# Performance work log

Measured on AMD Instinct MI355X. Metric: run time of the kernel, lower is better.

The kernel has to match this reference:

```python
import jax, jax.numpy as jnp
import numpy as np

P, N, C_IN = 30000, 64, 4     # pillars, max points per pillar, raw point features
OUT = 64                      # PFN output channels (must equal N for the original BN call)
C_AUG = C_IN + 5              # +3 cluster offsets, +2 center offsets
VX, VY = 0.2, 0.2
X_OFF = VX / 2 + 0.0          # pc_range x_min = 0
Y_OFF = VY / 2 + (-40.0)      # pc_range y_min = -40
EPS = 1e-3                    # BatchNorm eps from change_default_args


def setup_inputs() -> dict:
    key = jax.random.key(0)
    k1, k2, k3, k4, k5, k6 = jax.random.split(key, 6)
    features = jax.random.normal(k1, (P, N, C_IN), jnp.float32)
    num_points = jax.random.randint(k2, (P,), 1, N + 1, jnp.int32)  # >=1 to avoid div-by-zero
    coors = jax.random.randint(k3, (P, 4), 0, 352, jnp.int32)
    W = jax.random.normal(k4, (OUT, C_AUG), jnp.float32) * 0.1      # Linear(bias=False)
    gamma = 1.0 + 0.1 * jax.random.normal(k5, (OUT,), jnp.float32)  # BN weight
    beta = 0.1 * jax.random.normal(k6, (OUT,), jnp.float32)         # BN bias
    return {"features": features, "num_points": num_points, "coors": coors,
            "W": W, "gamma": gamma, "beta": beta}


def reference(features, num_points, coors, W, gamma, beta):
    dt = features.dtype
    npts = num_points.astype(dt)[:, None, None]                     # [P,1,1]
    xyz = features[:, :, :3]
    points_mean = xyz.sum(axis=1, keepdims=True) / npts             # [P,1,3]
    f_cluster = xyz - points_mean                                   # [P,N,3]
    cx = features[:, :, 0] - (coors[:, 3].astype(dt)[:, None] * VX + X_OFF)
    cy = features[:, :, 1] - (coors[:, 2].astype(dt)[:, None] * VY + Y_OFF)
    f_center = jnp.stack([cx, cy], axis=-1)                         # [P,N,2]
    feat = jnp.concatenate([features, f_cluster, f_center], axis=-1)  # [P,N,9]
    mask = (num_points[:, None] > jnp.arange(N, dtype=num_points.dtype))  # [P,N]
    feat = feat * mask[..., None].astype(dt)
    x = jnp.einsum('pnc,oc->pno', feat, W)                          # [P,N,OUT]
    # Faithful to the original: BatchNorm1d(OUT) applied WITHOUT permute, so the
    # channel axis is dim=1 (size N == OUT); training-mode batch stats over (P, last).
    mu = x.mean(axis=(0, 2), keepdims=True)                         # [1,N,1]
    var = x.var(axis=(0, 2), keepdims=True)                         # biased var, as BN
    x = (x - mu) * jax.lax.rsqrt(var + EPS) * gamma[None, :, None] + beta[None, :, None]
    x = jax.nn.relu(x)
    return x.max(axis=1)                                            # [P,OUT] (squeeze of keepdim max)
```

## Files before the change

kernel.cpp:

```cpp
#include <hip/hip_runtime.h>
#include <hip/hip_bf16.h>
#include <math.h>

typedef __attribute__((ext_vector_type(8))) __bf16 bf16x8;
typedef __attribute__((ext_vector_type(4))) float f32x4;

constexpr float VX_ = 0.2f;
constexpr float VY_ = 0.2f;
constexpr float X_OFF_ = 0.1f;
constexpr float Y_OFF_ = -39.9f;
constexpr float EPS_ = 1e-3f;

__device__ __forceinline__ float wave_sum(float v) {
#pragma unroll
  for (int off = 32; off; off >>= 1) v += __shfl_xor(v, off);
  return v;
}

__device__ __forceinline__ ushort bf16bits(float x) {
  __hip_bfloat16 h = __float2bfloat16(x);
  return __builtin_bit_cast(ushort, h);
}

__device__ __forceinline__ uint32_t cvtpk(float lo, float hi) {
  uint32_t r;
  asm("v_cvt_pk_bf16_f32 %0, %1, %2" : "=v"(r) : "v"(lo), "v"(hi));
  return r;
}

__global__ __launch_bounds__(256) void k0_prep(const float* __restrict__ W,
                                               float* __restrict__ gws,
                                               uint32_t* __restrict__ Bpack) {
  const int t = threadIdx.x;
  if (t < 180) {
    const int pr = t >> 2, k = t & 3;
    int c = 0, rem = pr;
    while (rem >= 9 - c) {
      rem -= 9 - c;
      ++c;
    }
    const int c2 = c + rem;
    float s = 0.f;
    for (int o = k * 16; o < k * 16 + 16; ++o) s += W[o * 9 + c] * W[o * 9 + c2];
    s += __shfl_xor(s, 1);
    s += __shfl_xor(s, 2);
    if (k == 0) gws[pr] = (c == c2) ? s : 2.f * s;
  } else if (t < 216) {
    const int tt = t - 180, c = tt >> 2, k = tt & 3;
    float s = 0.f;
    for (int o = k * 16; o < k * 16 + 16; ++o) s += W[o * 9 + c];
    s += __shfl_xor(s, 1);
    s += __shfl_xor(s, 2);
    if (k == 0) gws[45 + c] = s;
  }
  {
    const int nt = t >> 6, lane = t & 63;
    const int l16 = lane & 15, g16 = lane >> 4;
    const int col = nt * 16 + l16;
    ushort h[8];
#pragma unroll
    for (int j = 0; j < 8; ++j) {
      const int kk = 8 * g16 + j;
      h[j] = (kk < 9) ? bf16bits(W[col * 9 + kk]) : (ushort)0;
    }
    uint4 q;
    q.x = (uint)h[0] | ((uint)h[1] << 16);
    q.y = (uint)h[2] | ((uint)h[3] << 16);
    q.z = (uint)h[4] | ((uint)h[5] << 16);
    q.w = (uint)h[6] | ((uint)h[7] << 16);
    *reinterpret_cast<uint4*>(Bpack + (size_t)t * 4) = q;
  }
}

__global__ __launch_bounds__(256) void k1_moments(
    const float* __restrict__ feats, const int* __restrict__ npts_arr,
    const int* __restrict__ coors, const float* __restrict__ gwsbuf,
    float* __restrict__ partials, float* __restrict__ aux, int S, int P) {
  __shared__ float2 red[4][64];
  const int t = threadIdx.x, lane = t & 63, wv = t >> 6;
  float g[45], wsv[9];
#pragma unroll
  for (int i = 0; i < 45; ++i) g[i] = gwsbuf[i];
#pragma unroll
  for (int i = 0; i < 9; ++i) wsv[i] = gwsbuf[45 + i];

  float s1 = 0.f, s2 = 0.f;
  const int nw = S * 4;
  int p = blockIdx.x * 4 + wv;
  if (p < P) {
    float4 f =
        *reinterpret_cast<const float4*>(feats + (size_t)p * 256 + lane * 4);
    int np = npts_arr[p];
    int cx = coors[p * 4 + 3], cy = coors[p * 4 + 2];
    while (true) {
      const int p2 = p + nw;
      const bool has2 = p2 < P;
      float4 f2 = make_float4(0.f, 0.f, 0.f, 0.f);
      int np2 = 1, cx2 = 0, cy2 = 0;
      if (has2) {
        f2 = *reinterpret_cast<const float4*>(feats + (size_t)p2 * 256 +
                                              lane * 4);
        np2 = npts_arr[p2];
        cx2 = coors[p2 * 4 + 3];
        cy2 = coors[p2 * 4 + 2];
      }
      const float ox = (float)cx * VX_ + X_OFF_;
      const float oy = (float)cy * VY_ + Y_OFF_;
      const float inv = 1.f / (float)np;
      const float m0 = wave_sum(f.x) * inv;
      const float m1 = wave_sum(f.y) * inv;
      const float m2 = wave_sum(f.z) * inv;
      if (lane == 0) {
        *reinterpret_cast<float4*>(aux + (size_t)p * 8) =
            make_float4(m0, m1, m2, ox);
        *reinterpret_cast<float4*>(aux + (size_t)p * 8 + 4) =
            make_float4(oy, __int_as_float(np), 0.f, 0.f);
      }
      const bool valid = lane < np;
      float ft[9] = {f.x,      f.y,      f.z,      f.w,      f.x - m0,
                     f.y - m1, f.z - m2, f.x - ox, f.y - oy};
#pragma unroll
      for (int c = 0; c < 9; ++c) ft[c] = valid ? ft[c] : 0.f;
      int idx = 0;
      float t1 = 0.f, t2 = 0.f;
#pragma unroll
      for (int c = 0; c < 9; ++c) {
        float u = 0.f;
#pragma unroll
        for (int c2 = c; c2 < 9; ++c2) u = fmaf(g[idx++], ft[c2], u);
        t2 = fmaf(ft[c], u, t2);
        t1 = fmaf(ft[c], wsv[c], t1);
      }
      s1 += t1;
      s2 += t2;
      if (!has2) break;
      p = p2;
      f = f2;
      np = np2;
      cx = cx2;
      cy = cy2;
    }
  }
  red[wv][lane] = make_float2(s1, s2);
  __syncthreads();
  if (t < 64) {
    const float v = red[0][t].x + red[1][t].x + red[2][t].x + red[3][t].x;
    partials[((size_t)t * 2 + 0) * S + blockIdx.x] = v;
  } else if (t < 128) {
    const int n = t - 64;
    const float v = red[0][n].y + red[1][n].y + red[2][n].y + red[3][n].y;
    partials[((size_t)n * 2 + 1) * S + blockIdx.x] = v;
  }
}

__global__ __launch_bounds__(256) void k2_stats(
    const float* __restrict__ partials, const float* __restrict__ gamma,
    const float* __restrict__ beta, float* __restrict__ ab, int S, int P) {
  const int n = blockIdx.x, t = threadIdx.x;
  __shared__ float r1[4], r2[4];
  const float* p1 = partials + ((size_t)n * 2 + 0) * S;
  const float* p2 = partials + ((size_t)n * 2 + 1) * S;
  float a1 = 0.f, a2 = 0.f;
  for (int b = t; b < S; b += 256) {
    a1 += p1[b];
    a2 += p2[b];
  }
  a1 = wave_sum(a1);
  a2 = wave_sum(a2);
  const int wv = t >> 6;
  if ((t & 63) == 0) {
    r1[wv] = a1;
    r2[wv] = a2;
  }
  __syncthreads();
  if (t == 0) {
    const float v2 = r1[0] + r1[1] + r1[2] + r1[3];
    const float v1 = r2[0] + r2[1] + r2[2] + r2[3];
    const float invPN = 1.f / ((float)P * 64.f);
    const float mu = v2 * invPN;
    const float var = v1 * invPN - mu * mu;
    const float a = gamma[n] * rsqrtf(var + EPS_);
    const float b = beta[n] - mu * a;
    ab[n] = a;
    ab[64 + n] = b;
  }
}

__global__ __launch_bounds__(256) void k4_mfma(
    const float* __restrict__ feats, const float* __restrict__ aux,
    const uint32_t* __restrict__ Bpack, const float* __restrict__ ab,
    float* __restrict__ out, int P) {
  __shared__ uint32_t A_lds[4][64][20];
  __shared__ float2 shab[64];
  const int t = threadIdx.x, lane = t & 63, wv = t >> 6;
  const int g16 = lane >> 4, l16 = lane & 15;
  if (t < 64) shab[t] = make_float2(ab[t], ab[64 + t]);

  uint4 bq[4];
#pragma unroll
  for (int nt = 0; nt < 4; ++nt)
    bq[nt] =
        *reinterpret_cast<const uint4*>(Bpack + ((size_t)nt * 64 + lane) * 4);

  A_lds[wv][lane][6] = 0u;
  A_lds[wv][lane][7] = 0u;
  *reinterpret_cast<uint4*>(&A_lds[wv][lane][8]) = make_uint4(0u, 0u, 0u, 0u);
  *reinterpret_cast<uint4*>(&A_lds[wv][lane][12]) = make_uint4(0u, 0u, 0u, 0u);
  __syncthreads();

  float ar[16], br[16];
#pragma unroll
  for (int i = 0; i < 16; ++i) {
    const int n = (i >> 2) * 16 + g16 * 4 + (i & 3);
    const float2 v = shab[n];
    ar[i] = v.x;
    br[i] = v.y;
  }

  const int stride = gridDim.x * 4;
  int p = blockIdx.x * 4 + wv;
  if (p >= P) return;
  float4 f = *reinterpret_cast<const float4*>(feats + (size_t)p * 256 + lane * 4);
  float4 a0 = *reinterpret_cast<const float4*>(aux + (size_t)p * 8);
  float4 a1 = *reinterpret_cast<const float4*>(aux + (size_t)p * 8 + 4);
  while (true) {
    const int p2 = p + stride;
    const bool has2 = p2 < P;
    float4 f2 = make_float4(0.f, 0.f, 0.f, 0.f);
    float4 a0b = make_float4(0.f, 0.f, 0.f, 0.f);
    float4 a1b = make_float4(0.f, 0.f, 0.f, 0.f);
    if (has2) {
      f2 = *reinterpret_cast<const float4*>(feats + (size_t)p2 * 256 + lane * 4);
      a0b = *reinterpret_cast<const float4*>(aux + (size_t)p2 * 8);
      a1b = *reinterpret_cast<const float4*>(aux + (size_t)p2 * 8 + 4);
    }
    const float m0 = a0.x, m1 = a0.y, m2 = a0.z, ox = a0.w, oy = a1.x;
    const int np = __float_as_int(a1.y);
    const bool valid = lane < np;
    const float v0 = valid ? f.x : 0.f;
    const float v1 = valid ? f.y : 0.f;
    const float v2 = valid ? f.z : 0.f;
    const float v3 = valid ? f.w : 0.f;
    const float v4 = valid ? f.x - m0 : 0.f;
    const float v5 = valid ? f.y - m1 : 0.f;
    const float v6 = valid ? f.z - m2 : 0.f;
    const float v7 = valid ? f.x - ox : 0.f;
    const float v8 = valid ? f.y - oy : 0.f;
    union {
      uint32_t u[6];
      uint4 q;
    } pk;
    pk.u[0] = cvtpk(v0, v1);
    pk.u[1] = cvtpk(v2, v3);
    pk.u[2] = cvtpk(v4, v5);
    pk.u[3] = cvtpk(v6, v7);
    pk.u[4] = cvtpk(v8, 0.f);
    *reinterpret_cast<uint4*>(&A_lds[wv][lane][0]) = pk.q;
    *reinterpret_cast<uint2*>(&A_lds[wv][lane][4]) = make_uint2(pk.u[4], 0u);

    bf16x8 afr[4];
#pragma unroll
    for (int mt = 0; mt < 4; ++mt) {
      afr[mt] =
          *reinterpret_cast<const bf16x8*>(&A_lds[wv][mt * 16 + l16][g16 * 4]);
    }
    const f32x4 accz = {0.f, 0.f, 0.f, 0.f};
    float mx[4] = {0.f, 0.f, 0.f, 0.f};
#pragma unroll
    for (int mt = 0; mt < 4; ++mt) {
      const bf16x8 a = afr[mt];
#pragma unroll
      for (int nt = 0; nt < 4; ++nt) {
        f32x4 acc4 = __builtin_amdgcn_mfma_f32_16x16x32_bf16(
            a, __builtin_bit_cast(bf16x8, bq[nt]), accz, 0, 0, 0);
#pragma unroll
        for (int r = 0; r < 4; ++r) {
          const float y = fmaf(acc4[r], ar[mt * 4 + r], br[mt * 4 + r]);
          mx[nt] = fmaxf(mx[nt], y);
        }
      }
    }
#pragma unroll
    for (int nt = 0; nt < 4; ++nt) {
      mx[nt] = fmaxf(mx[nt], __shfl_xor(mx[nt], 16));
      mx[nt] = fmaxf(mx[nt], __shfl_xor(mx[nt], 32));
    }
    const float outv =
        (g16 == 0) ? mx[0] : (g16 == 1) ? mx[1] : (g16 == 2) ? mx[2] : mx[3];
    out[(size_t)p * 64 + lane] = outv;
    if (!has2) break;
    p = p2;
    f = f2;
    a0 = a0b;
    a1 = a1b;
  }
}

extern "C" void kernel_launch(void* const* d_in, const int* in_sizes, int n_in,
                              void* d_out, int out_size, void* d_ws,
                              size_t ws_size, hipStream_t stream) {
  const float* feats = (const float*)d_in[0];
  const int* npts = (const int*)d_in[1];
  const int* coors = (const int*)d_in[2];
  const float* W = (const float*)d_in[3];
  const float* gamma = (const float*)d_in[4];
  const float* beta = (const float*)d_in[5];
  float* out = (float*)d_out;
  float* ws = (float*)d_ws;

  const int P = in_sizes[1];

  float* gws = ws;
  uint32_t* Bpack = (uint32_t*)(ws + 64);
  float* ab = ws + 64 + 1024;
  float* aux = ws + 1216;
  float* partials = ws + 1216 + 8 * (size_t)P;

  int S = 2048;
  while (S > 1 &&
         (size_t)(64 * 2 * (size_t)S + 1216 + 8 * (size_t)P) * 4 > ws_size)
    S >>= 1;

  k0_prep<<<1, 256, 0, stream>>>(W, gws, Bpack);
  k1_moments<<<S, 256, 0, stream>>>(feats, npts, coors, gws, partials, aux, S,
                                    P);
  k2_stats<<<64, 256, 0, stream>>>(partials, gamma, beta, ab, S, P);
  const int g4 = (P + 15) / 16;
  k4_mfma<<<g4, 256, 0, stream>>>(feats, aux, Bpack, ab, out, P);
}
```

Measured before the change: 44.14 us.

## Fuse weight prep into moments kernel, shrink grid, one pillar per wave

Removes the single-block k0_prep launch by having every k1_moments block compute the Gram/weight-sum terms in LDS from W, with block 0 also writing the packed bf16 B matrix. The moments grid is fixed at 512 blocks instead of up to 2048, which reduces the partials that k2 has to reduce. k4 drops its grid-stride prefetch loop and launches one pillar per wave (P/4 blocks). Each block now redundantly recomputes the small W products, and the non-persistent k4 loses its load prefetching.

```diff
diff --git a/kernel.cpp b/kernel.cpp
--- a/kernel.cpp
+++ b/kernel.cpp
@@ -11,6 +11,8 @@
 constexpr float Y_OFF_ = -39.9f;
 constexpr float EPS_ = 1e-3f;
 
+#define S1 512
+
 __device__ __forceinline__ float wave_sum(float v) {
 #pragma unroll
   for (int off = 32; off; off >>= 1) v += __shfl_xor(v, off);
@@ -28,10 +30,18 @@
   return r;
 }
 
-__global__ __launch_bounds__(256) void k0_prep(const float* __restrict__ W,
-                                               float* __restrict__ gws,
-                                               uint32_t* __restrict__ Bpack) {
-  const int t = threadIdx.x;
+__global__ __launch_bounds__(256) void k1_moments(
+    const float* __restrict__ feats, const int* __restrict__ npts_arr,
+    const int* __restrict__ coors, const float* __restrict__ W,
+    float* __restrict__ partials, float* __restrict__ aux,
+    uint32_t* __restrict__ Bpack, int P) {
+  __shared__ float W_lds[576];
+  __shared__ float gws[54];
+  __shared__ float2 red[4][64];
+  const int t = threadIdx.x, lane = t & 63, wv = t >> 6;
+
+  for (int i = t; i < 576; i += 256) W_lds[i] = W[i];
+  __syncthreads();
   if (t < 180) {
     const int pr = t >> 2, k = t & 3;
     int c = 0, rem = pr;
@@ -41,27 +51,35 @@
     }
     const int c2 = c + rem;
     float s = 0.f;
-    for (int o = k * 16; o < k * 16 + 16; ++o) s += W[o * 9 + c] * W[o * 9 + c2];
+    for (int o = k * 16; o < k * 16 + 16; ++o)
+      s += W_lds[o * 9 + c] * W_lds[o * 9 + c2];
     s += __shfl_xor(s, 1);
     s += __shfl_xor(s, 2);
     if (k == 0) gws[pr] = (c == c2) ? s : 2.f * s;
   } else if (t < 216) {
     const int tt = t - 180, c = tt >> 2, k = tt & 3;
     float s = 0.f;
-    for (int o = k * 16; o < k * 16 + 16; ++o) s += W[o * 9 + c];
+    for (int o = k * 16; o < k * 16 + 16; ++o) s += W_lds[o * 9 + c];
     s += __shfl_xor(s, 1);
     s += __shfl_xor(s, 2);
     if (k == 0) gws[45 + c] = s;
   }
-  {
-    const int nt = t >> 6, lane = t & 63;
-    const int l16 = lane & 15, g16 = lane >> 4;
+  __syncthreads();
+  float g[45], wsv[9];
+#pragma unroll
+  for (int i = 0; i < 45; ++i) g[i] = gws[i];
+#pragma unroll
+  for (int i = 0; i < 9; ++i) wsv[i] = gws[45 + i];
+
+  if (blockIdx.x == 0) {
+    const int nt = t >> 6, bl = t & 63;
+    const int l16 = bl & 15, g16 = bl >> 4;
     const int col = nt * 16 + l16;
     ushort h[8];
 #pragma unroll
     for (int j = 0; j < 8; ++j) {
       const int kk = 8 * g16 + j;
-      h[j] = (kk < 9) ? bf16bits(W[col * 9 + kk]) : (ushort)0;
+      h[j] = (kk < 9) ? bf16bits(W_lds[col * 9 + kk]) : (ushort)0;
     }
     uint4 q;
     q.x = (uint)h[0] | ((uint)h[1] << 16);
@@ -70,22 +88,9 @@
     q.w = (uint)h[6] | ((uint)h[7] << 16);
     *reinterpret_cast<uint4*>(Bpack + (size_t)t * 4) = q;
   }
-}
-
-__global__ __launch_bounds__(256) void k1_moments(
-    const float* __restrict__ feats, const int* __restrict__ npts_arr,
-    const int* __restrict__ coors, const float* __restrict__ gwsbuf,
-    float* __restrict__ partials, float* __restrict__ aux, int S, int P) {
-  __shared__ float2 red[4][64];
-  const int t = threadIdx.x, lane = t & 63, wv = t >> 6;
-  float g[45], wsv[9];
-#pragma unroll
-  for (int i = 0; i < 45; ++i) g[i] = gwsbuf[i];
-#pragma unroll
-  for (int i = 0; i < 9; ++i) wsv[i] = gwsbuf[45 + i];
 
   float s1 = 0.f, s2 = 0.f;
-  const int nw = S * 4;
+  const int nw = S1 * 4;
   int p = blockIdx.x * 4 + wv;
   if (p < P) {
     float4 f =
@@ -145,23 +150,23 @@
   __syncthreads();
   if (t < 64) {
     const float v = red[0][t].x + red[1][t].x + red[2][t].x + red[3][t].x;
-    partials[((size_t)t * 2 + 0) * S + blockIdx.x] = v;
+    partials[((size_t)t * 2 + 0) * S1 + blockIdx.x] = v;
   } else if (t < 128) {
     const int n = t - 64;
     const float v = red[0][n].y + red[1][n].y + red[2][n].y + red[3][n].y;
-    partials[((size_t)n * 2 + 1) * S + blockIdx.x] = v;
+    partials[((size_t)n * 2 + 1) * S1 + blockIdx.x] = v;
   }
 }
 
 __global__ __launch_bounds__(256) void k2_stats(
     const float* __restrict__ partials, const float* __restrict__ gamma,
-    const float* __restrict__ beta, float* __restrict__ ab, int S, int P) {
+    const float* __restrict__ beta, float* __restrict__ ab, int P) {
   const int n = blockIdx.x, t = threadIdx.x;
   __shared__ float r1[4], r2[4];
-  const float* p1 = partials + ((size_t)n * 2 + 0) * S;
-  const float* p2 = partials + ((size_t)n * 2 + 1) * S;
+  const float* p1 = partials + ((size_t)n * 2 + 0) * S1;
+  const float* p2 = partials + ((size_t)n * 2 + 1) * S1;
   float a1 = 0.f, a2 = 0.f;
-  for (int b = t; b < S; b += 256) {
+  for (int b = t; b < S1; b += 256) {
     a1 += p1[b];
     a2 += p2[b];
   }
@@ -217,83 +222,67 @@
     br[i] = v.y;
   }
 
-  const int stride = gridDim.x * 4;
-  int p = blockIdx.x * 4 + wv;
+  const int p = blockIdx.x * 4 + wv;
   if (p >= P) return;
-  float4 f = *reinterpret_cast<const float4*>(feats + (size_t)p * 256 + lane * 4);
-  float4 a0 = *reinterpret_cast<const float4*>(aux + (size_t)p * 8);
-  float4 a1 = *reinterpret_cast<const float4*>(aux + (size_t)p * 8 + 4);
-  while (true) {
-    const int p2 = p + stride;
-    const bool has2 = p2 < P;
-    float4 f2 = make_float4(0.f, 0.f, 0.f, 0.f);
-    float4 a0b = make_float4(0.f, 0.f, 0.f, 0.f);
-    float4 a1b = make_float4(0.f, 0.f, 0.f, 0.f);
-    if (has2) {
-      f2 = *reinterpret_cast<const float4*>(feats + (size_t)p2 * 256 + lane * 4);
-      a0b = *reinterpret_cast<const float4*>(aux + (size_t)p2 * 8);
-      a1b = *reinterpret_cast<const float4*>(aux + (size_t)p2 * 8 + 4);
-    }
-    const float m0 = a0.x, m1 = a0.y, m2 = a0.z, ox = a0.w, oy = a1.x;
-    const int np = __float_as_int(a1.y);
-    const bool valid = lane < np;
-    const float v0 = valid ? f.x : 0.f;
-    const float v1 = valid ? f.y : 0.f;
-    const float v2 = valid ? f.z : 0.f;
-    const float v3 = valid ? f.w : 0.f;
-    const float v4 = valid ? f.x - m0 : 0.f;
-    const float v5 = valid ? f.y - m1 : 0.f;
-    const float v6 = valid ? f.z - m2 : 0.f;
-    const float v7 = valid ? f.x - ox : 0.f;
-    const float v8 = valid ? f.y - oy : 0.f;
-    union {
-      uint32_t u[6];
-      uint4 q;
-    } pk;
-    pk.u[0] = cvtpk(v0, v1);
-    pk.u[1] = cvtpk(v2, v3);
-    pk.u[2] = cvtpk(v4, v5);
-    pk.u[3] = cvtpk(v6, v7);
-    pk.u[4] = cvtpk(v8, 0.f);
-    *reinterpret_cast<uint4*>(&A_lds[wv][lane][0]) = pk.q;
-    *reinterpret_cast<uint2*>(&A_lds[wv][lane][4]) = make_uint2(pk.u[4], 0u);
-
-    bf16x8 afr[4];
-#pragma unroll
-    for (int mt = 0; mt < 4; ++mt) {
-      afr[mt] =
-          *reinterpret_cast<const bf16x8*>(&A_lds[wv][mt * 16 + l16][g16 * 4]);
-    }
-    const f32x4 accz = {0.f, 0.f, 0.f, 0.f};
-    float mx[4] = {0.f, 0.f, 0.f, 0.f};
-#pragma unroll
-    for (int mt = 0; mt < 4; ++mt) {
-      const bf16x8 a = afr[mt];
-#pragma unroll
-      for (int nt = 0; nt < 4; ++nt) {
-        f32x4 acc4 = __builtin_amdgcn_mfma_f32_16x16x32_bf16(
-            a, __builtin_bit_cast(bf16x8, bq[nt]), accz, 0, 0, 0);
-#pragma unroll
-        for (int r = 0; r < 4; ++r) {
-          const float y = fmaf(acc4[r], ar[mt * 4 + r], br[mt * 4 + r]);
-          mx[nt] = fmaxf(mx[nt], y);
-        }
+  const float4 f =
+      *reinterpret_cast<const float4*>(feats + (size_t)p * 256 + lane * 4);
+  const float4 a0 = *reinterpret_cast<const float4*>(aux + (size_t)p * 8);
+  const float4 a1 = *reinterpret_cast<const float4*>(aux + (size_t)p * 8 + 4);
+
+  const float m0 = a0.x, m1 = a0.y, m2 = a0.z, ox = a0.w, oy = a1.x;
+  const int np = __float_as_int(a1.y);
+  const bool valid = lane < np;
+  const float v0 = valid ? f.x : 0.f;
+  const float v1 = valid ? f.y : 0.f;
+  const float v2 = valid ? f.z : 0.f;
+  const float v3 = valid ? f.w : 0.f;
+  const float v4 = valid ? f.x - m0 : 0.f;
+  const float v5 = valid ? f.y - m1 : 0.f;
+  const float v6 = valid ? f.z - m2 : 0.f;
+  const float v7 = valid ? f.x - ox : 0.f;
+  const float v8 = valid ? f.y - oy : 0.f;
+  union {
+    uint32_t u[6];
+    uint4 q;
+  } pk;
+  pk.u[0] = cvtpk(v0, v1);
+  pk.u[1] = cvtpk(v2, v3);
+  pk.u[2] = cvtpk(v4, v5);
+  pk.u[3] = cvtpk(v6, v7);
+  pk.u[4] = cvtpk(v8, 0.f);
+  *reinterpret_cast<uint4*>(&A_lds[wv][lane][0]) = pk.q;
+  *reinterpret_cast<uint2*>(&A_lds[wv][lane][4]) = make_uint2(pk.u[4], 0u);
+
+  bf16x8 afr[4];
+#pragma unroll
+  for (int mt = 0; mt < 4; ++mt) {
+    afr[mt] =
+        *reinterpret_cast<const bf16x8*>(&A_lds[wv][mt * 16 + l16][g16 * 4]);
+  }
+  const f32x4 accz = {0.f, 0.f, 0.f, 0.f};
+  float mx[4] = {0.f, 0.f, 0.f, 0.f};
+#pragma unroll
+  for (int mt = 0; mt < 4; ++mt) {
+    const bf16x8 a = afr[mt];
+#pragma unroll
+    for (int nt = 0; nt < 4; ++nt) {
+      f32x4 acc4 = __builtin_amdgcn_mfma_f32_16x16x32_bf16(
+          a, __builtin_bit_cast(bf16x8, bq[nt]), accz, 0, 0, 0);
+#pragma unroll
+      for (int r = 0; r < 4; ++r) {
+        const float y = fmaf(acc4[r], ar[mt * 4 + r], br[mt * 4 + r]);
+        mx[nt] = fmaxf(mx[nt], y);
       }
     }
-#pragma unroll
-    for (int nt = 0; nt < 4; ++nt) {
-      mx[nt] = fmaxf(mx[nt], __shfl_xor(mx[nt], 16));
-      mx[nt] = fmaxf(mx[nt], __shfl_xor(mx[nt], 32));
-    }
-    const float outv =
-        (g16 == 0) ? mx[0] : (g16 == 1) ? mx[1] : (g16 == 2) ? mx[2] : mx[3];
-    out[(size_t)p * 64 + lane] = outv;
-    if (!has2) break;
-    p = p2;
-    f = f2;
-    a0 = a0b;
-    a1 = a1b;
-  }
+  }
+#pragma unroll
+  for (int nt = 0; nt < 4; ++nt) {
+    mx[nt] = fmaxf(mx[nt], __shfl_xor(mx[nt], 16));
+    mx[nt] = fmaxf(mx[nt], __shfl_xor(mx[nt], 32));
+  }
+  const float outv =
+      (g16 == 0) ? mx[0] : (g16 == 1) ? mx[1] : (g16 == 2) ? mx[2] : mx[3];
+  out[(size_t)p * 64 + lane] = outv;
 }
 
 extern "C" void kernel_launch(void* const* d_in, const int* in_sizes, int n_in,
@@ -310,21 +299,14 @@
 
   const int P = in_sizes[1];
 
-  float* gws = ws;
-  uint32_t* Bpack = (uint32_t*)(ws + 64);
-  float* ab = ws + 64 + 1024;
-  float* aux = ws + 1216;
-  float* partials = ws + 1216 + 8 * (size_t)P;
-
-  int S = 2048;
-  while (S > 1 &&
-         (size_t)(64 * 2 * (size_t)S + 1216 + 8 * (size_t)P) * 4 > ws_size)
-    S >>= 1;
-
-  k0_prep<<<1, 256, 0, stream>>>(W, gws, Bpack);
-  k1_moments<<<S, 256, 0, stream>>>(feats, npts, coors, gws, partials, aux, S,
-                                    P);
-  k2_stats<<<64, 256, 0, stream>>>(partials, gamma, beta, ab, S, P);
-  const int g4 = (P + 15) / 16;
-  k4_mfma<<<g4, 256, 0, stream>>>(feats, aux, Bpack, ab, out, P);
-}
+  float* ab = ws;
+  uint32_t* Bpack = (uint32_t*)(ws + 128);
+  float* partials = ws + 128 + 1024;
+  float* aux = partials + 64 * 2 * S1;
+
+  k1_moments<<<S1, 256, 0, stream>>>(feats, npts, coors, W, partials, aux,
+                                     Bpack, P);
+  k2_stats<<<64, 256, 0, stream>>>(partials, gamma, beta, ab, P);
+  const int g1 = (P + 3) / 4;
+  k4_mfma<<<g1, 256, 0, stream>>>(feats, aux, Bpack, ab, out, P);
+}
```

Measured after the change: 42.87 us. -2.9%, faster.
